# Kernel optimization log

Hardware: AMD Instinct MI355X
Metric: run time of the kernel (lower is better)

The kernel has to match this reference:

```python
import jax, jax.numpy as jnp
import numpy as np

NT = 128          # num_timesteps (reference query points)
E = 128           # embed_time
H = 128           # nhidden
NH = 1            # num_heads
F = 32            # feature_size
NS = 2            # num_states
EPS = 1e-5


def layer_norm(x, g, b):
    m = jnp.mean(x, axis=-1, keepdims=True)
    v = jnp.mean((x - m) ** 2, axis=-1, keepdims=True)
    return (x - m) * jax.lax.rsqrt(v + EPS) * g + b


def setup_inputs() -> dict:
    key = jax.random.key(0)
    ks = jax.random.split(key, 24)
    nrm = lambda k, s: (jax.random.normal(k, s) * 0.05).astype(jnp.float32)
    inp = {
        "input": jax.random.normal(ks[0], (8, F, 512), dtype=jnp.float32),
        "mask": jax.random.randint(ks[1], (8, F, 512), 0, 2).astype(jnp.float32),
        "timesteps": jnp.sort(jax.random.uniform(ks[2], (8, 512), dtype=jnp.float32), axis=-1),
        # time embedding
        "periodic_w": nrm(ks[3], (E - 1, 1)), "periodic_b": nrm(ks[4], (E - 1,)),
        "lin_w": nrm(ks[5], (1, 1)), "lin_b": nrm(ks[6], (1,)),
        # query / key projections + layer norms
        "q_w": nrm(ks[7], (E, E)), "q_b": nrm(ks[8], (E,)),
        "q_g": jnp.ones((E,), jnp.float32), "q_be": jnp.zeros((E,), jnp.float32),
        "k_w": nrm(ks[9], (E, E)), "k_b": nrm(ks[10], (E,)),
        "k_g": jnp.ones((E,), jnp.float32), "k_be": jnp.zeros((E,), jnp.float32),
        # attention_norm over h*2F channels, then output linear + LN to nhidden
        "attn_g": jnp.ones((NH * 2 * F,), jnp.float32), "attn_b": jnp.zeros((NH * 2 * F,), jnp.float32),
        "out_w": nrm(ks[11], (H, NH * 2 * F)), "out_b": nrm(ks[12], (H,)),
        "out_g": jnp.ones((H,), jnp.float32), "out_be": jnp.zeros((H,), jnp.float32),
        # GRU (torch gate order r, z, n)
        "gru_wih": nrm(ks[13], (3 * H, H)), "gru_whh": nrm(ks[14], (3 * H, H)),
        "gru_bih": nrm(ks[15], (3 * H,)), "gru_bhh": nrm(ks[16], (3 * H,)),
        # classifier MLP
        "c1_w": nrm(ks[17], (H, H)), "c1_b": nrm(ks[18], (H,)),
        "c2_w": nrm(ks[19], (H, H)), "c2_b": nrm(ks[20], (H,)),
        "c3_w": nrm(ks[21], (NS, H)), "c3_b": nrm(ks[22], (NS,)),
    }
    return inp


def time_embedding(tt, lin_w, lin_b, periodic_w, periodic_b):
    t = tt[..., None]                                   # (..., 1)
    out1 = t @ lin_w.T + lin_b                          # (..., 1)
    out2 = jnp.sin(t @ periodic_w.T + periodic_b)       # (..., E-1)
    return jnp.concatenate([out1, out2], axis=-1)       # (..., E)


def reference(input, mask, timesteps, periodic_w, periodic_b, lin_w, lin_b,
              q_w, q_b, q_g, q_be, k_w, k_b, k_g, k_be,
              attn_g, attn_b, out_w, out_b, out_g, out_be,
              gru_wih, gru_whh, gru_bih, gru_bhh,
              c1_w, c1_b, c2_w, c2_b, c3_w, c3_b):
    B = input.shape[0]
    x_in = jnp.transpose(input, (0, 2, 1))              # (B, T, F)
    m = 1.0 - jnp.transpose(mask, (0, 2, 1))            # (B, T, F)
    x_in = x_in * (m > 0).astype(x_in.dtype)
    x = jnp.concatenate([x_in, m], axis=-1)             # (B, T, 2F)
    mk = jnp.concatenate([m, m], axis=-1)               # (B, T, 2F)

    key_e = time_embedding(timesteps, lin_w, lin_b, periodic_w, periodic_b)        # (B, T, E)
    qtimes = jnp.linspace(0.0, 1.0, NT)
    query_e = time_embedding(qtimes[None], lin_w, lin_b, periodic_w, periodic_b)   # (1, NT, E)

    q = layer_norm(query_e @ q_w.T + q_b, q_g, q_be)    # (1, NT, E)
    k = layer_norm(key_e @ k_w.T + k_b, k_g, k_be)      # (B, T, E)

    etk = E // NH
    q = q.reshape(1, NT, NH, etk).transpose(0, 2, 1, 3)         # (1, h, NT, etk)
    k = k.reshape(B, -1, NH, etk).transpose(0, 2, 1, 3)         # (B, h, T, etk)

    scores = jnp.einsum("ahqd,bhkd->bhqk", q, k) / np.sqrt(etk)  # (B, h, NT, T)
    # per-channel masked softmax over keys: (B, h, NT, T, 2F)
    logits = jnp.where(mk[:, None, None, :, :] == 0, -1e9, scores[..., None])
    p_attn = jax.nn.softmax(logits, axis=-2)
    att = jnp.sum(p_attn * x[:, None, None, :, :], axis=-2)     # (B, h, NT, 2F)

    x2 = att.transpose(0, 2, 1, 3).reshape(B, NT, NH * 2 * F)
    x2 = layer_norm(x2, attn_g, attn_b)
    out = layer_norm(x2 @ out_w.T + out_b, out_g, out_be)       # (B, NT, H)

    # GRU over the NT reference timesteps, last hidden state
    seq = out.transpose(1, 0, 2)                                # (NT, B, H)
    h0 = jnp.zeros((B, H), out.dtype)

    def gru_step(h, x_t):
        gi = x_t @ gru_wih.T + gru_bih
        gh = h @ gru_whh.T + gru_bhh
        ir, iz, inn = jnp.split(gi, 3, axis=-1)
        hr, hz, hn = jnp.split(gh, 3, axis=-1)
        r = jax.nn.sigmoid(ir + hr)
        z = jax.nn.sigmoid(iz + hz)
        n = jnp.tanh(inn + r * hn)
        h_new = (1.0 - z) * n + z * h
        return h_new, None

    h_last, _ = jax.lax.scan(gru_step, h0, seq)

    h1 = jax.nn.relu(h_last @ c1_w.T + c1_b)
    h2 = jax.nn.relu(h1 @ c2_w.T + c2_b)
    return h2 @ c3_w.T + c3_b                                   # (B, num_states) logits
```

## Files before the change

kernel.cpp:

```cpp
#include <hip/hip_runtime.h>
#include <math.h>

#define LN_EPS 1e-5f

typedef _Float16 h2v __attribute__((ext_vector_type(2)));

__device__ __forceinline__ float dot4(float4 a, float4 b) {
    return a.x*b.x + a.y*b.y + a.z*b.z + a.w*b.w;
}
__device__ __forceinline__ void fma4(float4& a, float s, float4 v) {
    a.x += s*v.x; a.y += s*v.y; a.z += s*v.z; a.w += s*v.w;
}
__device__ __forceinline__ float fast_rcp(float x) {
    return __builtin_amdgcn_rcpf(x);
}
__device__ __forceinline__ float fast_sigmoid(float x) {
    return fast_rcp(1.f + __expf(-x));
}
__device__ __forceinline__ float fast_tanh(float x) {
    return 1.f - 2.f*fast_rcp(__expf(2.f*x) + 1.f);
}
__device__ __forceinline__ float fdot2u(unsigned int a, unsigned int b, float c) {
#if __has_builtin(__builtin_amdgcn_fdot2)
    return __builtin_amdgcn_fdot2(__builtin_bit_cast(h2v, a),
                                  __builtin_bit_cast(h2v, b), c, false);
#else
    const h2v av = __builtin_bit_cast(h2v, a);
    const h2v bv = __builtin_bit_cast(h2v, b);
    return c + (float)av[0]*(float)bv[0] + (float)av[1]*(float)bv[1];
#endif
}
__device__ __forceinline__ float wsum64(float v) {
    #pragma unroll
    for (int off = 32; off > 0; off >>= 1) v += __shfl_xor(v, off);
    return v;
}

__global__ void k_embed_proj(
    const float* __restrict__ input, const float* __restrict__ mask,
    const float* __restrict__ timesteps,
    const float* __restrict__ pw, const float* __restrict__ pb,
    const float* __restrict__ lw, const float* __restrict__ lb,
    const float* __restrict__ q_w, const float* __restrict__ q_b,
    const float* __restrict__ q_g, const float* __restrict__ q_be,
    const float* __restrict__ k_w, const float* __restrict__ k_b,
    const float* __restrict__ k_g, const float* __restrict__ k_be,
    float* __restrict__ qs, float* __restrict__ kT, float2* __restrict__ xm)
{
    const int blk = blockIdx.x;
    const int tid = threadIdx.x;

    __shared__ __align__(16) float e[4][128];
    __shared__ __align__(16) float4 red[128];
    __shared__ __align__(16) float proj[4][128];
    __shared__ __align__(16) float2 tile[32][65];

    if (blk < 64) {
        const int b  = blk >> 3;
        const int t0 = (blk & 7) * 64;
        const int cg = tid >> 6;
        const int tt = tid & 63;
        #pragma unroll
        for (int c16 = 0; c16 < 16; ++c16) {
            const int c = c16*2 + cg;
            const float m = mask [(size_t)(b*32 + c)*512 + t0 + tt];
            const float x = input[(size_t)(b*32 + c)*512 + t0 + tt];
            const float mm = 1.0f - m;
            tile[c][tt] = make_float2(x*mm, mm);
        }
        __syncthreads();
        const int c2 = tid & 31;
        const int tg = tid >> 5;
        #pragma unroll
        for (int k = 0; k < 16; ++k) {
            const int t = tg*16 + k;
            xm[((size_t)b*512 + t0 + t)*32 + c2] = tile[c2][t];
        }
        return;
    }

    const bool isq = blk < 96;
    float tv[4];
    int kidx0 = 0;
    if (isq) {
        const int q0 = (blk - 64) * 4;
        #pragma unroll
        for (int r = 0; r < 4; ++r) tv[r] = (float)(q0 + r) * (1.0f/127.0f);
    } else {
        kidx0 = (blk - 96) * 4;
        #pragma unroll
        for (int r = 0; r < 4; ++r) tv[r] = timesteps[kidx0 + r];
    }

    float pwj = 0.f, pbj = 0.f;
    if (tid > 0) { pwj = pw[tid-1]; pbj = pb[tid-1]; }
    const float lw0 = lw[0], lb0 = lb[0];
    #pragma unroll
    for (int r = 0; r < 4; ++r)
        e[r][tid] = (tid == 0) ? (tv[r]*lw0 + lb0) : sinf(tv[r]*pwj + pbj);
    __syncthreads();

    const float* W  = isq ? q_w  : k_w;
    const float* Bv = isq ? q_b  : k_b;
    const float* G  = isq ? q_g  : k_g;
    const float* Be = isq ? q_be : k_be;

    {
        const int jj = tid >> 2, dc = tid & 3;
        const float4* e0 = (const float4*)(&e[0][0]);
        const float4* e1 = (const float4*)(&e[1][0]);
        const float4* e2 = (const float4*)(&e[2][0]);
        const float4* e3 = (const float4*)(&e[3][0]);
        #pragma unroll
        for (int jb = 0; jb < 4; ++jb) {
            const int j = jb*32 + jj;
            const float4* wrow = (const float4*)(W + (size_t)j*128);
            float a0=0.f, a1=0.f, a2=0.f, a3=0.f;
            #pragma unroll
            for (int k = 0; k < 8; ++k) {
                const int idx = dc + 4*k;
                const float4 w4 = wrow[idx];
                a0 += dot4(w4, e0[idx]);
                a1 += dot4(w4, e1[idx]);
                a2 += dot4(w4, e2[idx]);
                a3 += dot4(w4, e3[idx]);
            }
            a0 += __shfl_xor(a0, 1, 4); a0 += __shfl_xor(a0, 2, 4);
            a1 += __shfl_xor(a1, 1, 4); a1 += __shfl_xor(a1, 2, 4);
            a2 += __shfl_xor(a2, 1, 4); a2 += __shfl_xor(a2, 2, 4);
            a3 += __shfl_xor(a3, 1, 4); a3 += __shfl_xor(a3, 2, 4);
            if (dc == 0) {
                const float bj = Bv[j];
                proj[0][j] = a0 + bj; proj[1][j] = a1 + bj;
                proj[2][j] = a2 + bj; proj[3][j] = a3 + bj;
            }
        }
    }
    __syncthreads();

    float acc[4];
    #pragma unroll
    for (int r = 0; r < 4; ++r) acc[r] = proj[r][tid];

    red[tid] = make_float4(acc[0], acc[1], acc[2], acc[3]);
    __syncthreads();
    for (int s = 64; s > 0; s >>= 1) {
        if (tid < s) {
            float4 m = red[tid]; const float4 o = red[tid+s];
            m.x += o.x; m.y += o.y; m.z += o.z; m.w += o.w;
            red[tid] = m;
        }
        __syncthreads();
    }
    float4 mean = red[0];
    mean.x *= (1.0f/128.0f); mean.y *= (1.0f/128.0f);
    mean.z *= (1.0f/128.0f); mean.w *= (1.0f/128.0f);
    __syncthreads();
    const float d0 = acc[0]-mean.x, d1 = acc[1]-mean.y,
                d2 = acc[2]-mean.z, d3 = acc[3]-mean.w;
    red[tid] = make_float4(d0*d0, d1*d1, d2*d2, d3*d3);
    __syncthreads();
    for (int s = 64; s > 0; s >>= 1) {
        if (tid < s) {
            float4 m = red[tid]; const float4 o = red[tid+s];
            m.x += o.x; m.y += o.y; m.z += o.z; m.w += o.w;
            red[tid] = m;
        }
        __syncthreads();
    }
    float4 var = red[0];
    var.x *= (1.0f/128.0f); var.y *= (1.0f/128.0f);
    var.z *= (1.0f/128.0f); var.w *= (1.0f/128.0f);

    const float gg = G[tid], bb = Be[tid];
    const float o0 = d0*rsqrtf(var.x+LN_EPS)*gg + bb;
    const float o1 = d1*rsqrtf(var.y+LN_EPS)*gg + bb;
    const float o2 = d2*rsqrtf(var.z+LN_EPS)*gg + bb;
    const float o3 = d3*rsqrtf(var.w+LN_EPS)*gg + bb;

    if (isq) {
        const float sc = 0.08838834764831845f;
        const int q0 = (blk - 64)*4;
        qs[(size_t)(q0+0)*128 + tid] = o0*sc;
        qs[(size_t)(q0+1)*128 + tid] = o1*sc;
        qs[(size_t)(q0+2)*128 + tid] = o2*sc;
        qs[(size_t)(q0+3)*128 + tid] = o3*sc;
    } else {
        const int b = kidx0 >> 9;
        const int t = kidx0 & 511;
        *(float4*)(kT + ((size_t)(b*128 + tid))*512 + t) =
            make_float4(o0, o1, o2, o3);
    }
}

__global__ void __launch_bounds__(256) k_attn(
    const float2* __restrict__ xm,
    const float* __restrict__ qs, const float* __restrict__ kT,
    const float* __restrict__ attn_g, const float* __restrict__ attn_b,
    const float* __restrict__ out_w, const float* __restrict__ out_b,
    const float* __restrict__ out_g, const float* __restrict__ out_be,
    float* __restrict__ outm)
{
    const int b     = blockIdx.x >> 5;
    const int qbase = (blockIdx.x & 31) * 4;
    const int tid   = threadIdx.x;

    __shared__ __align__(16) float et[4][512];
    __shared__ __align__(16) float qsh[4][128];
    __shared__ __align__(16) float wsh[128*66];
    __shared__ __align__(16) float sA[4][8][32];
    __shared__ __align__(16) float aA[4][8][32];
    __shared__ __align__(16) float x2s[4][64];
    __shared__ float redC[4];

    for (int idx = tid; idx < 512; idx += 256)
        qsh[idx >> 7][idx & 127] = qs[(size_t)(qbase + (idx >> 7))*128 + (idx & 127)];
    for (int idx = tid; idx < 8192; idx += 256)
        wsh[(idx >> 6)*66 + (idx & 63)] = out_w[idx];
    __syncthreads();

    {
        const int grp = tid >> 7;
        const int tl  = tid & 127;
        const int q0  = grp*2;
        const float4* kp  = (const float4*)kT + (size_t)b*128*128 + tl;
        const float4* qa4 = (const float4*)qsh[q0];
        const float4* qb4 = (const float4*)qsh[q0+1];
        float4 a0 = make_float4(0,0,0,0), a1 = make_float4(0,0,0,0);
        float4 c0 = kp[0], c1 = kp[128], c2 = kp[256], c3 = kp[384];
        for (int c = 0; c < 32; ++c) {
            float4 n0, n1, n2, n3;
            if (c < 31) {
                const float4* kn = kp + (size_t)(4*c+4)*128;
                n0 = kn[0]; n1 = kn[128]; n2 = kn[256]; n3 = kn[384];
            }
            const float4 qa = qa4[c], qb = qb4[c];
            fma4(a0, qa.x, c0); fma4(a1, qb.x, c0);
            fma4(a0, qa.y, c1); fma4(a1, qb.y, c1);
            fma4(a0, qa.z, c2); fma4(a1, qb.z, c2);
            fma4(a0, qa.w, c3); fma4(a1, qb.w, c3);
            c0 = n0; c1 = n1; c2 = n2; c3 = n3;
        }
        a0.x = __expf(a0.x); a0.y = __expf(a0.y); a0.z = __expf(a0.z); a0.w = __expf(a0.w);
        a1.x = __expf(a1.x); a1.y = __expf(a1.y); a1.z = __expf(a1.z); a1.w = __expf(a1.w);
        ((float4*)et[q0])[tl]   = a0;
        ((float4*)et[q0+1])[tl] = a1;
    }
    __syncthreads();

    {
        const int c   = tid & 31;
        const int seg = tid >> 5;
        const float2* xp = xm + ((size_t)b*512 + seg*64)*32 + c;
        float s0=0,s1=0,s2=0,s3=0, a0=0,a1=0,a2=0,a3=0;
        #pragma unroll 4
        for (int i = 0; i < 64; ++i) {
            const float2 v = xp[(size_t)i*32];
            const int t = seg*64 + i;
            const float w0 = et[0][t]*v.y, w1 = et[1][t]*v.y;
            const float w2 = et[2][t]*v.y, w3 = et[3][t]*v.y;
            s0 += w0; s1 += w1; s2 += w2; s3 += w3;
            a0 += w0*v.x; a1 += w1*v.x; a2 += w2*v.x; a3 += w3*v.x;
        }
        sA[0][seg][c]=s0; sA[1][seg][c]=s1; sA[2][seg][c]=s2; sA[3][seg][c]=s3;
        aA[0][seg][c]=a0; aA[1][seg][c]=a1; aA[2][seg][c]=a2; aA[3][seg][c]=a3;
    }
    __syncthreads();

    {
        const int ql = tid >> 6;
        const int c2 = tid & 63;
        const int cc = c2 & 31;
        float ss = 0.f;
        #pragma unroll
        for (int g = 0; g < 8; ++g) ss += sA[ql][g][cc];
        float attv;
        if (c2 < 32) {
            float aa = 0.f;
            #pragma unroll
            for (int g = 0; g < 8; ++g) aa += aA[ql][g][cc];
            attv = (ss > 0.f) ? aa/ss : 0.f;
        } else {
            attv = (ss > 0.f) ? 1.0f : 0.0f;
        }
        const float mean = wsum64(attv) * (1.0f/64.0f);
        const float dv = attv - mean;
        const float var = wsum64(dv*dv) * (1.0f/64.0f);
        x2s[ql][c2] = dv*rsqrtf(var+LN_EPS)*attn_g[c2] + attn_b[c2];
    }
    __syncthreads();

    {
        const int jhalf = tid >> 7;
        const int j     = tid & 127;
        const int wave  = tid >> 6;
        for (int lq2 = 0; lq2 < 2; ++lq2) {
            const int ql = jhalf*2 + lq2;
            float acc = out_b[j];
            const float4* wrow = (const float4*)(wsh + j*66);
            const float4* xr   = (const float4*)x2s[ql];
            #pragma unroll
            for (int k = 0; k < 16; ++k) acc += dot4(wrow[k], xr[k]);

            float v = wsum64(acc);
            if ((tid & 63) == 0) redC[wave] = v;
            __syncthreads();
            const float mean = (redC[jhalf*2] + redC[jhalf*2+1]) * (1.0f/128.0f);
            __syncthreads();
            const float d = acc - mean;
            v = wsum64(d*d);
            if ((tid & 63) == 0) redC[wave] = v;
            __syncthreads();
            const float var = (redC[jhalf*2] + redC[jhalf*2+1]) * (1.0f/128.0f);
            outm[((size_t)b*128 + qbase + ql)*128 + j] =
                d*rsqrtf(var+LN_EPS)*out_g[j] + out_be[j];
            __syncthreads();
        }
    }
}

__global__ void k_gi(const float* __restrict__ outm,
                     const float* __restrict__ wih, const float* __restrict__ bih,
                     float* __restrict__ gi)
{
    const int qi  = blockIdx.x;
    const int tid = threadIdx.x;
    __shared__ __align__(16) float rows[8][128];
    for (int idx = tid; idx < 1024; idx += 384) {
        const int b = idx >> 7, d = idx & 127;
        rows[b][d] = outm[(size_t)(b*128+qi)*128 + d];
    }
    __syncthreads();

    const int g0 = tid >> 2, dc = tid & 3;
    #pragma unroll
    for (int gb = 0; gb < 4; ++gb) {
        const int g = gb*96 + g0;
        const float4* wrow = (const float4*)(wih + (size_t)g*128);
        float acc[8] = {0,0,0,0,0,0,0,0};
        #pragma unroll
        for (int k = 0; k < 8; ++k) {
            const int idx = dc + 4*k;
            const float4 w4 = wrow[idx];
            #pragma unroll
            for (int b = 0; b < 8; ++b)
                acc[b] += dot4(w4, ((const float4*)rows[b])[idx]);
        }
        #pragma unroll
        for (int b = 0; b < 8; ++b) {
            acc[b] += __shfl_xor(acc[b], 1, 4);
            acc[b] += __shfl_xor(acc[b], 2, 4);
        }
        if (dc == 0) {
            const float bi = bih[g];
            #pragma unroll
            for (int b = 0; b < 8; ++b)
                gi[((size_t)qi*8 + b)*384 + g] = acc[b] + bi;
        }
    }
}

__global__ void __launch_bounds__(512) k_gru_cls(
    const float* __restrict__ gi,
    const float* __restrict__ whh, const float* __restrict__ bhh,
    const float* __restrict__ c1w, const float* __restrict__ c1b,
    const float* __restrict__ c2w, const float* __restrict__ c2b,
    const float* __restrict__ c3w, const float* __restrict__ c3b,
    float* __restrict__ out)
{
    const int b   = blockIdx.x;
    const int tid = threadIdx.x;
    const int s   = tid >> 7;
    const int u   = tid & 127;

    __shared__ __align__(16) unsigned int lds[25344];
    unsigned int* hP = lds;
    float4* part4 = (float4*)&lds[64];
    float* hcls = (float*)&lds[64 + 1536];

    {
        const float4* w4 = (const float4*)whh;
        #pragma unroll 4
        for (int k = 0; k < 24; ++k) {
            const int idx = tid + k*512;
            const float4 v = w4[idx];
            const int row = idx >> 5, c4 = idx & 31;
            h2v p0; p0[0] = (_Float16)v.x; p0[1] = (_Float16)v.y;
            h2v p1; p1[0] = (_Float16)v.z; p1[1] = (_Float16)v.w;
            lds[row*66 + c4*2    ] = __builtin_bit_cast(unsigned int, p0);
            lds[row*66 + c4*2 + 1] = __builtin_bit_cast(unsigned int, p1);
        }
    }
    __syncthreads();

    unsigned int wreg[3][16];
    #pragma unroll
    for (int g = 0; g < 3; ++g) {
        const uint2* src = (const uint2*)&lds[(g*128 + u)*66 + 16*s];
        #pragma unroll
        for (int i = 0; i < 8; ++i) {
            const uint2 t = src[i];
            wreg[g][2*i] = t.x; wreg[g][2*i+1] = t.y;
        }
    }
    __syncthreads();

    const float* gbase = gi + (size_t)b*384;
    float bh_r=0.f, bh_z=0.f, bh_n=0.f, gr0=0.f, gz0=0.f, gn0=0.f, hprev=0.f;
    if (tid < 64) hP[tid] = 0u;
    if (s == 0) {
        bh_r = bhh[u]; bh_z = bhh[u+128]; bh_n = bhh[u+256];
        gr0 = gbase[u]; gz0 = gbase[u+128]; gn0 = gbase[u+256];
    }
    __syncthreads();

    for (int qi = 0; qi < 128; ++qi) {
        const uint4* hp4 = (const uint4*)hP + s*4;
        float ar = 0.f, az = 0.f, an = 0.f;
        #pragma unroll
        for (int i = 0; i < 4; ++i) {
            const uint4 hv = hp4[i];
            ar = fdot2u(wreg[0][4*i+0], hv.x, ar);
            ar = fdot2u(wreg[0][4*i+1], hv.y, ar);
            ar = fdot2u(wreg[0][4*i+2], hv.z, ar);
            ar = fdot2u(wreg[0][4*i+3], hv.w, ar);
            az = fdot2u(wreg[1][4*i+0], hv.x, az);
            az = fdot2u(wreg[1][4*i+1], hv.y, az);
            az = fdot2u(wreg[1][4*i+2], hv.z, az);
            az = fdot2u(wreg[1][4*i+3], hv.w, az);
            an = fdot2u(wreg[2][4*i+0], hv.x, an);
            an = fdot2u(wreg[2][4*i+1], hv.y, an);
            an = fdot2u(wreg[2][4*i+2], hv.z, an);
            an = fdot2u(wreg[2][4*i+3], hv.w, an);
        }
        if (s > 0) part4[(s-1)*128 + u] = make_float4(ar, az, an, 0.f);

        float grn=0.f, gzn=0.f, gnn=0.f;
        if (s == 0 && qi < 127) {
            const float* gb = gbase + (size_t)(qi+1)*3072;
            grn = gb[u]; gzn = gb[u+128]; gnn = gb[u+256];
        }
        __syncthreads();

        if (s == 0) {
            const float4 p0 = part4[u], p1 = part4[128+u], p2 = part4[256+u];
            const float ghr = ar + p0.x + p1.x + p2.x + bh_r;
            const float ghz = az + p0.y + p1.y + p2.y + bh_z;
            const float ghn = an + p0.z + p1.z + p2.z + bh_n;
            const float r = fast_sigmoid(gr0 + ghr);
            const float z = fast_sigmoid(gz0 + ghz);
            const float n = fast_tanh(gn0 + r*ghn);
            const float hn2 = (1.f - z)*n + z*hprev;
            hprev = hn2;
            gr0 = grn; gz0 = gzn; gn0 = gnn;
            const float other = __shfl_xor(hn2, 1);
            if ((u & 1) == 0) {
                h2v hp; hp[0] = (_Float16)hn2; hp[1] = (_Float16)other;
                hP[u >> 1] = __builtin_bit_cast(unsigned int, hp);
            }
        }
        __syncthreads();
    }

    float* scr = (float*)part4;
    if (s == 0) hcls[u] = hprev;
    __syncthreads();
    if (tid < 128) {
        float acc = c1b[u];
        const float4* wc = (const float4*)(c1w + (size_t)u*128);
        const float4* v  = (const float4*)hcls;
        #pragma unroll
        for (int d4 = 0; d4 < 32; ++d4) acc += dot4(wc[d4], v[d4]);
        scr[u] = fmaxf(acc, 0.f);
    }
    __syncthreads();
    if (tid < 128) {
        float acc = c2b[u];
        const float4* wc = (const float4*)(c2w + (size_t)u*128);
        const float4* v  = (const float4*)scr;
        #pragma unroll
        for (int d4 = 0; d4 < 32; ++d4) acc += dot4(wc[d4], v[d4]);
        scr[128 + u] = fmaxf(acc, 0.f);
    }
    __syncthreads();
    if (tid < 2) {
        float acc = c3b[tid];
        const float4* wc = (const float4*)(c3w + (size_t)tid*128);
        const float4* v  = (const float4*)(scr + 128);
        #pragma unroll
        for (int d4 = 0; d4 < 32; ++d4) acc += dot4(wc[d4], v[d4]);
        out[(size_t)b*2 + tid] = acc;
    }
}

extern "C" void kernel_launch(void* const* d_in, const int* in_sizes, int n_in,
                              void* d_out, int out_size, void* d_ws, size_t ws_size,
                              hipStream_t stream)
{
    const float* input     = (const float*)d_in[0];
    const float* mask      = (const float*)d_in[1];
    const float* timesteps = (const float*)d_in[2];
    const float* pw        = (const float*)d_in[3];
    const float* pb        = (const float*)d_in[4];
    const float* lw        = (const float*)d_in[5];
    const float* lb        = (const float*)d_in[6];
    const float* q_w       = (const float*)d_in[7];
    const float* q_b       = (const float*)d_in[8];
    const float* q_g       = (const float*)d_in[9];
    const float* q_be      = (const float*)d_in[10];
    const float* k_w       = (const float*)d_in[11];
    const float* k_b       = (const float*)d_in[12];
    const float* k_g       = (const float*)d_in[13];
    const float* k_be      = (const float*)d_in[14];
    const float* attn_g    = (const float*)d_in[15];
    const float* attn_b    = (const float*)d_in[16];
    const float* out_w     = (const float*)d_in[17];
    const float* out_b     = (const float*)d_in[18];
    const float* out_g     = (const float*)d_in[19];
    const float* out_be    = (const float*)d_in[20];
    const float* gru_wih   = (const float*)d_in[21];
    const float* gru_whh   = (const float*)d_in[22];
    const float* gru_bih   = (const float*)d_in[23];
    const float* gru_bhh   = (const float*)d_in[24];
    const float* c1_w      = (const float*)d_in[25];
    const float* c1_b      = (const float*)d_in[26];
    const float* c2_w      = (const float*)d_in[27];
    const float* c2_b      = (const float*)d_in[28];
    const float* c3_w      = (const float*)d_in[29];
    const float* c3_b      = (const float*)d_in[30];

    float* ws   = (float*)d_ws;
    float*  qs   = ws;
    float*  kT   = qs   + 16384;
    float*  outm = kT   + 524288;
    float*  gi   = outm + 131072;
    float2* xm   = (float2*)(gi + 393216);

    k_embed_proj<<<1120, 128, 0, stream>>>(input, mask, timesteps,
                                           pw, pb, lw, lb,
                                           q_w, q_b, q_g, q_be,
                                           k_w, k_b, k_g, k_be, qs, kT, xm);
    k_attn<<<256, 256, 0, stream>>>(xm, qs, kT,
                                    attn_g, attn_b, out_w, out_b,
                                    out_g, out_be, outm);
    k_gi<<<128, 384, 0, stream>>>(outm, gru_wih, gru_bih, gi);
    k_gru_cls<<<8, 512, 0, stream>>>(gi, gru_whh, gru_bhh,
                                     c1_w, c1_b, c2_w, c2_b, c3_w, c3_b,
                                     (float*)d_out);
}
```

Baseline: 240.5 us.

## Run GRU recurrence with one thread per hidden unit and double-buffered state

```diff
diff --git a/kernel.cpp b/kernel.cpp
--- a/kernel.cpp
+++ b/kernel.cpp
@@ -360,7 +360,7 @@
     }
 }
 
-__global__ void __launch_bounds__(512) k_gru_cls(
+__global__ void __launch_bounds__(128) k_gru_cls(
     const float* __restrict__ gi,
     const float* __restrict__ whh, const float* __restrict__ bhh,
     const float* __restrict__ c1w, const float* __restrict__ c1b,
@@ -368,21 +368,19 @@
     const float* __restrict__ c3w, const float* __restrict__ c3b,
     float* __restrict__ out)
 {
-    const int b   = blockIdx.x;
-    const int tid = threadIdx.x;
-    const int s   = tid >> 7;
-    const int u   = tid & 127;
+    const int b = blockIdx.x;
+    const int u = threadIdx.x;
 
     __shared__ __align__(16) unsigned int lds[25344];
-    unsigned int* hP = lds;
-    float4* part4 = (float4*)&lds[64];
-    float* hcls = (float*)&lds[64 + 1536];
+    unsigned int* hP  = lds;
+    float* hcls = (float*)&lds[192];
+    float* scr  = (float*)&lds[320];
 
     {
         const float4* w4 = (const float4*)whh;
         #pragma unroll 4
-        for (int k = 0; k < 24; ++k) {
-            const int idx = tid + k*512;
+        for (int k = 0; k < 96; ++k) {
+            const int idx = u + k*128;
             const float4 v = w4[idx];
             const int row = idx >> 5, c4 = idx & 31;
             h2v p0; p0[0] = (_Float16)v.x; p0[1] = (_Float16)v.y;
@@ -393,79 +391,70 @@
     }
     __syncthreads();
 
-    unsigned int wreg[3][16];
-    #pragma unroll
-    for (int g = 0; g < 3; ++g) {
-        const uint2* src = (const uint2*)&lds[(g*128 + u)*66 + 16*s];
-        #pragma unroll
-        for (int i = 0; i < 8; ++i) {
-            const uint2 t = src[i];
-            wreg[g][2*i] = t.x; wreg[g][2*i+1] = t.y;
+    unsigned int wr_[64], wz_[64], wn_[64];
+    {
+        const uint2* sr = (const uint2*)&lds[(size_t)u*66];
+        const uint2* sz = (const uint2*)&lds[(size_t)(u+128)*66];
+        const uint2* sn = (const uint2*)&lds[(size_t)(u+256)*66];
+        #pragma unroll
+        for (int i = 0; i < 32; ++i) {
+            const uint2 a = sr[i]; wr_[2*i] = a.x; wr_[2*i+1] = a.y;
+            const uint2 c = sz[i]; wz_[2*i] = c.x; wz_[2*i+1] = c.y;
+            const uint2 d = sn[i]; wn_[2*i] = d.x; wn_[2*i+1] = d.y;
         }
     }
     __syncthreads();
 
     const float* gbase = gi + (size_t)b*384;
-    float bh_r=0.f, bh_z=0.f, bh_n=0.f, gr0=0.f, gz0=0.f, gn0=0.f, hprev=0.f;
-    if (tid < 64) hP[tid] = 0u;
-    if (s == 0) {
-        bh_r = bhh[u]; bh_z = bhh[u+128]; bh_n = bhh[u+256];
-        gr0 = gbase[u]; gz0 = gbase[u+128]; gn0 = gbase[u+256];
-    }
-    __syncthreads();
-
+    const float bh_r = bhh[u], bh_z = bhh[u+128], bh_n = bhh[u+256];
+    float gr0 = gbase[u], gz0 = gbase[u+128], gn0 = gbase[u+256];
+    float hprev = 0.f;
+    if (u < 64) hP[u] = 0u;
+    __syncthreads();
+
+    int p = 0;
     for (int qi = 0; qi < 128; ++qi) {
-        const uint4* hp4 = (const uint4*)hP + s*4;
+        const uint4* hp4 = (const uint4*)(hP + p*64);
         float ar = 0.f, az = 0.f, an = 0.f;
         #pragma unroll
-        for (int i = 0; i < 4; ++i) {
+        for (int i = 0; i < 16; ++i) {
             const uint4 hv = hp4[i];
-            ar = fdot2u(wreg[0][4*i+0], hv.x, ar);
-            ar = fdot2u(wreg[0][4*i+1], hv.y, ar);
-            ar = fdot2u(wreg[0][4*i+2], hv.z, ar);
-            ar = fdot2u(wreg[0][4*i+3], hv.w, ar);
-            az = fdot2u(wreg[1][4*i+0], hv.x, az);
-            az = fdot2u(wreg[1][4*i+1], hv.y, az);
-            az = fdot2u(wreg[1][4*i+2], hv.z, az);
-            az = fdot2u(wreg[1][4*i+3], hv.w, az);
-            an = fdot2u(wreg[2][4*i+0], hv.x, an);
-            an = fdot2u(wreg[2][4*i+1], hv.y, an);
-            an = fdot2u(wreg[2][4*i+2], hv.z, an);
-            an = fdot2u(wreg[2][4*i+3], hv.w, an);
-        }
-        if (s > 0) part4[(s-1)*128 + u] = make_float4(ar, az, an, 0.f);
-
-        float grn=0.f, gzn=0.f, gnn=0.f;
-        if (s == 0 && qi < 127) {
+            ar = fdot2u(wr_[4*i+0], hv.x, ar);
+            ar = fdot2u(wr_[4*i+1], hv.y, ar);
+            ar = fdot2u(wr_[4*i+2], hv.z, ar);
+            ar = fdot2u(wr_[4*i+3], hv.w, ar);
+            az = fdot2u(wz_[4*i+0], hv.x, az);
+            az = fdot2u(wz_[4*i+1], hv.y, az);
+            az = fdot2u(wz_[4*i+2], hv.z, az);
+            az = fdot2u(wz_[4*i+3], hv.w, az);
+            an = fdot2u(wn_[4*i+0], hv.x, an);
+            an = fdot2u(wn_[4*i+1], hv.y, an);
+            an = fdot2u(wn_[4*i+2], hv.z, an);
+            an = fdot2u(wn_[4*i+3], hv.w, an);
+        }
+
+        float grn = 0.f, gzn = 0.f, gnn = 0.f;
+        if (qi < 127) {
             const float* gb = gbase + (size_t)(qi+1)*3072;
             grn = gb[u]; gzn = gb[u+128]; gnn = gb[u+256];
         }
+
+        const float r = fast_sigmoid(gr0 + ar + bh_r);
+        const float z = fast_sigmoid(gz0 + az + bh_z);
+        const float n = fast_tanh(gn0 + r*(an + bh_n));
+        const float hn2 = (1.f - z)*n + z*hprev;
+        hprev = hn2;
+        gr0 = grn; gz0 = gzn; gn0 = gnn;
+
+        _Float16* hw = (_Float16*)(hP + (1-p)*64);
+        hw[u] = (_Float16)hn2;
         __syncthreads();
-
-        if (s == 0) {
-            const float4 p0 = part4[u], p1 = part4[128+u], p2 = part4[256+u];
-            const float ghr = ar + p0.x + p1.x + p2.x + bh_r;
-            const float ghz = az + p0.y + p1.y + p2.y + bh_z;
-            const float ghn = an + p0.z + p1.z + p2.z + bh_n;
-            const float r = fast_sigmoid(gr0 + ghr);
-            const float z = fast_sigmoid(gz0 + ghz);
-            const float n = fast_tanh(gn0 + r*ghn);
-            const float hn2 = (1.f - z)*n + z*hprev;
-            hprev = hn2;
-            gr0 = grn; gz0 = gzn; gn0 = gnn;
-            const float other = __shfl_xor(hn2, 1);
-            if ((u & 1) == 0) {
-                h2v hp; hp[0] = (_Float16)hn2; hp[1] = (_Float16)other;
-                hP[u >> 1] = __builtin_bit_cast(unsigned int, hp);
-            }
-        }
-        __syncthreads();
-    }
-
-    float* scr = (float*)part4;
-    if (s == 0) hcls[u] = hprev;
-    __syncthreads();
-    if (tid < 128) {
+        p ^= 1;
+    }
+
+    hcls[u] = hprev;
+    __syncthreads();
+    {
         float acc = c1b[u];
         const float4* wc = (const float4*)(c1w + (size_t)u*128);
         const float4* v  = (const float4*)hcls;
@@ -474,7 +463,7 @@
         scr[u] = fmaxf(acc, 0.f);
     }
     __syncthreads();
-    if (tid < 128) {
+    {
         float acc = c2b[u];
         const float4* wc = (const float4*)(c2w + (size_t)u*128);
         const float4* v  = (const float4*)scr;
@@ -483,13 +472,13 @@
         scr[128 + u] = fmaxf(acc, 0.f);
     }
     __syncthreads();
-    if (tid < 2) {
-        float acc = c3b[tid];
-        const float4* wc = (const float4*)(c3w + (size_t)tid*128);
+    if (u < 2) {
+        float acc = c3b[u];
+        const float4* wc = (const float4*)(c3w + (size_t)u*128);
         const float4* v  = (const float4*)(scr + 128);
         #pragma unroll
         for (int d4 = 0; d4 < 32; ++d4) acc += dot4(wc[d4], v[d4]);
-        out[(size_t)b*2 + tid] = acc;
+        out[(size_t)b*2 + u] = acc;
     }
 }
 
@@ -544,7 +533,7 @@
                                     attn_g, attn_b, out_w, out_b,
                                     out_g, out_be, outm);
     k_gi<<<128, 384, 0, stream>>>(outm, gru_wih, gru_bih, gi);
-    k_gru_cls<<<8, 512, 0, stream>>>(gi, gru_whh, gru_bhh,
+    k_gru_cls<<<8, 128, 0, stream>>>(gi, gru_whh, gru_bhh,
                                      c1_w, c1_b, c2_w, c2_b, c3_w, c3_b,
                                      (float*)d_out);
 }
```

Measured after the change: 248.8 us. +3.5%, slower.

## Prefetch all GRU input-gate values into LDS as fp16 before the recurrence

Applied to the files above, without the earlier changes.

```diff
diff --git a/kernel.cpp b/kernel.cpp
--- a/kernel.cpp
+++ b/kernel.cpp
@@ -29,6 +29,10 @@
     const h2v bv = __builtin_bit_cast(h2v, b);
     return c + (float)av[0]*(float)bv[0] + (float)av[1]*(float)bv[1];
 #endif
+}
+__device__ __forceinline__ float half_of(unsigned int w, int hi) {
+    const h2v p = __builtin_bit_cast(h2v, w);
+    return (float)p[hi];
 }
 __device__ __forceinline__ float wsum64(float v) {
     #pragma unroll
@@ -373,10 +377,9 @@
     const int s   = tid >> 7;
     const int u   = tid & 127;
 
-    __shared__ __align__(16) unsigned int lds[25344];
-    unsigned int* hP = lds;
-    float4* part4 = (float4*)&lds[64];
-    float* hcls = (float*)&lds[64 + 1536];
+    __shared__ __align__(16) unsigned int lds[25984];
+    unsigned int* hP    = lds + 24384;
+    float4*       part4 = (float4*)(lds + 24448);
 
     {
         const float4* w4 = (const float4*)whh;
@@ -405,15 +408,27 @@
     }
     __syncthreads();
 
+    {
+        const float* gb0 = gi;
+        for (int idx = tid; idx < 24384; idx += 512) {
+            const int q1 = idx / 192;
+            const int pr = idx - q1*192;
+            const float2 v = *(const float2*)(gb0 +
+                ((size_t)(q1+1)*8 + b)*384 + 2*pr);
+            h2v pk; pk[0] = (_Float16)v.x; pk[1] = (_Float16)v.y;
+            lds[idx] = __builtin_bit_cast(unsigned int, pk);
+        }
+    }
     const float* gbase = gi + (size_t)b*384;
     float bh_r=0.f, bh_z=0.f, bh_n=0.f, gr0=0.f, gz0=0.f, gn0=0.f, hprev=0.f;
-    if (tid < 64) hP[tid] = 0u;
-    if (s == 0) {
+    if (tid < 128) {
         bh_r = bhh[u]; bh_z = bhh[u+128]; bh_n = bhh[u+256];
         gr0 = gbase[u]; gz0 = gbase[u+128]; gn0 = gbase[u+256];
     }
-    __syncthreads();
-
+    if (tid < 64) hP[tid] = 0u;
+    __syncthreads();
+
+    const int uh = u >> 1, up = u & 1;
     for (int qi = 0; qi < 128; ++qi) {
         const uint4* hp4 = (const uint4*)hP + s*4;
         float ar = 0.f, az = 0.f, an = 0.f;
@@ -436,13 +451,15 @@
         if (s > 0) part4[(s-1)*128 + u] = make_float4(ar, az, an, 0.f);
 
         float grn=0.f, gzn=0.f, gnn=0.f;
-        if (s == 0 && qi < 127) {
-            const float* gb = gbase + (size_t)(qi+1)*3072;
-            grn = gb[u]; gzn = gb[u+128]; gnn = gb[u+256];
+        if (tid < 128 && qi < 127) {
+            const unsigned int* gq = lds + (size_t)qi*192;
+            grn = half_of(gq[uh],       up);
+            gzn = half_of(gq[64 + uh],  up);
+            gnn = half_of(gq[128 + uh], up);
         }
         __syncthreads();
 
-        if (s == 0) {
+        if (tid < 128) {
             const float4 p0 = part4[u], p1 = part4[128+u], p2 = part4[256+u];
             const float ghr = ar + p0.x + p1.x + p2.x + bh_r;
             const float ghz = az + p0.y + p1.y + p2.y + bh_z;
@@ -453,17 +470,14 @@
             const float hn2 = (1.f - z)*n + z*hprev;
             hprev = hn2;
             gr0 = grn; gz0 = gzn; gn0 = gnn;
-            const float other = __shfl_xor(hn2, 1);
-            if ((u & 1) == 0) {
-                h2v hp; hp[0] = (_Float16)hn2; hp[1] = (_Float16)other;
-                hP[u >> 1] = __builtin_bit_cast(unsigned int, hp);
-            }
+            ((_Float16*)hP)[u] = (_Float16)hn2;
         }
         __syncthreads();
     }
 
-    float* scr = (float*)part4;
-    if (s == 0) hcls[u] = hprev;
+    float* hcls = (float*)lds;
+    float* scr  = (float*)lds + 128;
+    if (tid < 128) hcls[u] = hprev;
     __syncthreads();
     if (tid < 128) {
         float acc = c1b[u];
```

New measurement: 246.3 us. 2.4% more time.

## Pack GRU input gates as fp16 pairs and prefetch them into LDS

Applied to the files above, without the earlier changes.

```diff
diff --git a/kernel.cpp b/kernel.cpp
--- a/kernel.cpp
+++ b/kernel.cpp
@@ -29,6 +29,10 @@
     const h2v bv = __builtin_bit_cast(h2v, b);
     return c + (float)av[0]*(float)bv[0] + (float)av[1]*(float)bv[1];
 #endif
+}
+__device__ __forceinline__ float half_of(unsigned int w, int hi) {
+    const h2v p = __builtin_bit_cast(h2v, w);
+    return (float)p[hi];
 }
 __device__ __forceinline__ float wsum64(float v) {
     #pragma unroll
@@ -321,7 +325,7 @@
 
 __global__ void k_gi(const float* __restrict__ outm,
                      const float* __restrict__ wih, const float* __restrict__ bih,
-                     float* __restrict__ gi)
+                     unsigned int* __restrict__ gi3)
 {
     const int qi  = blockIdx.x;
     const int tid = threadIdx.x;
@@ -346,22 +350,30 @@
             for (int b = 0; b < 8; ++b)
                 acc[b] += dot4(w4, ((const float4*)rows[b])[idx]);
         }
+        const float bi = bih[g];
         #pragma unroll
         for (int b = 0; b < 8; ++b) {
             acc[b] += __shfl_xor(acc[b], 1, 4);
             acc[b] += __shfl_xor(acc[b], 2, 4);
-        }
-        if (dc == 0) {
-            const float bi = bih[g];
-            #pragma unroll
-            for (int b = 0; b < 8; ++b)
-                gi[((size_t)qi*8 + b)*384 + g] = acc[b] + bi;
-        }
-    }
-}
-
-__global__ void __launch_bounds__(512) k_gru_cls(
-    const float* __restrict__ gi,
+            acc[b] += bi;
+        }
+        const bool writer = (dc == 0) && ((g & 1) == 0);
+        const int v    = (g & 127) >> 1;
+        const int gate = g >> 7;
+        #pragma unroll
+        for (int b = 0; b < 8; ++b) {
+            const float pB = __shfl_xor(acc[b], 4);
+            if (writer) {
+                h2v pk; pk[0] = (_Float16)acc[b]; pk[1] = (_Float16)pB;
+                gi3[((size_t)qi*8 + b)*192 + v*3 + gate] =
+                    __builtin_bit_cast(unsigned int, pk);
+            }
+        }
+    }
+}
+
+__global__ void __launch_bounds__(256) k_gru_cls(
+    const unsigned int* __restrict__ gi3,
     const float* __restrict__ whh, const float* __restrict__ bhh,
     const float* __restrict__ c1w, const float* __restrict__ c1b,
     const float* __restrict__ c2w, const float* __restrict__ c2b,
@@ -370,125 +382,172 @@
 {
     const int b   = blockIdx.x;
     const int tid = threadIdx.x;
-    const int s   = tid >> 7;
-    const int u   = tid & 127;
-
-    __shared__ __align__(16) unsigned int lds[25344];
-    unsigned int* hP = lds;
-    float4* part4 = (float4*)&lds[64];
-    float* hcls = (float*)&lds[64 + 1536];
+    const int s   = tid >> 6;
+    const int v   = tid & 63;
+
+    __shared__ __align__(16) unsigned int lds[25984];
+    unsigned int* giL = lds;
+    unsigned int* hP  = lds + 24384;
+    float2* part2     = (float2*)(lds + 24448);
+    float* hcls       = (float*)(lds + 25600);
+    float* scr        = (float*)(lds + 25728);
 
     {
         const float4* w4 = (const float4*)whh;
         #pragma unroll 4
-        for (int k = 0; k < 24; ++k) {
-            const int idx = tid + k*512;
-            const float4 v = w4[idx];
+        for (int k = 0; k < 48; ++k) {
+            const int idx = tid + k*256;
+            const float4 val = w4[idx];
             const int row = idx >> 5, c4 = idx & 31;
-            h2v p0; p0[0] = (_Float16)v.x; p0[1] = (_Float16)v.y;
-            h2v p1; p1[0] = (_Float16)v.z; p1[1] = (_Float16)v.w;
+            h2v p0; p0[0] = (_Float16)val.x; p0[1] = (_Float16)val.y;
+            h2v p1; p1[0] = (_Float16)val.z; p1[1] = (_Float16)val.w;
             lds[row*66 + c4*2    ] = __builtin_bit_cast(unsigned int, p0);
             lds[row*66 + c4*2 + 1] = __builtin_bit_cast(unsigned int, p1);
         }
     }
     __syncthreads();
 
-    unsigned int wreg[3][16];
-    #pragma unroll
-    for (int g = 0; g < 3; ++g) {
-        const uint2* src = (const uint2*)&lds[(g*128 + u)*66 + 16*s];
-        #pragma unroll
-        for (int i = 0; i < 8; ++i) {
-            const uint2 t = src[i];
-            wreg[g][2*i] = t.x; wreg[g][2*i+1] = t.y;
-        }
-    }
-    __syncthreads();
-
-    const float* gbase = gi + (size_t)b*384;
-    float bh_r=0.f, bh_z=0.f, bh_n=0.f, gr0=0.f, gz0=0.f, gn0=0.f, hprev=0.f;
+    unsigned int w6[6][16];
+    {
+        const int rows6[6] = { 2*v, 2*v+1, 128+2*v, 129+2*v, 256+2*v, 257+2*v };
+        #pragma unroll
+        for (int r = 0; r < 6; ++r) {
+            const uint2* src = (const uint2*)&lds[rows6[r]*66 + s*16];
+            #pragma unroll
+            for (int i = 0; i < 8; ++i) {
+                const uint2 t = src[i];
+                w6[r][2*i] = t.x; w6[r][2*i+1] = t.y;
+            }
+        }
+    }
+    __syncthreads();
+
+    for (int idx = tid; idx < 24384; idx += 256) {
+        const int q1 = idx / 192;
+        const int j  = idx - q1*192;
+        giL[idx] = gi3[((size_t)(q1+1)*8 + b)*192 + j];
+    }
+
+    float bhrA=0.f,bhrB=0.f,bhzA=0.f,bhzB=0.f,bhnA=0.f,bhnB=0.f;
+    if (s == 1) {
+        bhrA = bhh[2*v];     bhrB = bhh[2*v+1];
+        bhzA = bhh[128+2*v]; bhzB = bhh[129+2*v];
+        bhnA = bhh[256+2*v]; bhnB = bhh[257+2*v];
+    }
+    unsigned int gu0=0u, gu1=0u, gu2=0u;
+    float hprevA = 0.f, hprevB = 0.f;
+    if (s == 0) {
+        const unsigned int* g0p = gi3 + (size_t)b*192 + v*3;
+        gu0 = g0p[0]; gu1 = g0p[1]; gu2 = g0p[2];
+    }
     if (tid < 64) hP[tid] = 0u;
-    if (s == 0) {
-        bh_r = bhh[u]; bh_z = bhh[u+128]; bh_n = bhh[u+256];
-        gr0 = gbase[u]; gz0 = gbase[u+128]; gn0 = gbase[u+256];
-    }
     __syncthreads();
 
     for (int qi = 0; qi < 128; ++qi) {
         const uint4* hp4 = (const uint4*)hP + s*4;
-        float ar = 0.f, az = 0.f, an = 0.f;
+        float arA=0.f, arB=0.f, azA=0.f, azB=0.f, anA=0.f, anB=0.f;
         #pragma unroll
         for (int i = 0; i < 4; ++i) {
             const uint4 hv = hp4[i];
-            ar = fdot2u(wreg[0][4*i+0], hv.x, ar);
-            ar = fdot2u(wreg[0][4*i+1], hv.y, ar);
-            ar = fdot2u(wreg[0][4*i+2], hv.z, ar);
-            ar = fdot2u(wreg[0][4*i+3], hv.w, ar);
-            az = fdot2u(wreg[1][4*i+0], hv.x, az);
-            az = fdot2u(wreg[1][4*i+1], hv.y, az);
-            az = fdot2u(wreg[1][4*i+2], hv.z, az);
-            az = fdot2u(wreg[1][4*i+3], hv.w, az);
-            an = fdot2u(wreg[2][4*i+0], hv.x, an);
-            an = fdot2u(wreg[2][4*i+1], hv.y, an);
-            an = fdot2u(wreg[2][4*i+2], hv.z, an);
-            an = fdot2u(wreg[2][4*i+3], hv.w, an);
-        }
-        if (s > 0) part4[(s-1)*128 + u] = make_float4(ar, az, an, 0.f);
-
-        float grn=0.f, gzn=0.f, gnn=0.f;
+            arA = fdot2u(w6[0][4*i+0], hv.x, arA);
+            arA = fdot2u(w6[0][4*i+1], hv.y, arA);
+            arA = fdot2u(w6[0][4*i+2], hv.z, arA);
+            arA = fdot2u(w6[0][4*i+3], hv.w, arA);
+            arB = fdot2u(w6[1][4*i+0], hv.x, arB);
+            arB = fdot2u(w6[1][4*i+1], hv.y, arB);
+            arB = fdot2u(w6[1][4*i+2], hv.z, arB);
+            arB = fdot2u(w6[1][4*i+3], hv.w, arB);
+            azA = fdot2u(w6[2][4*i+0], hv.x, azA);
+            azA = fdot2u(w6[2][4*i+1], hv.y, azA);
+            azA = fdot2u(w6[2][4*i+2], hv.z, azA);
+            azA = fdot2u(w6[2][4*i+3], hv.w, azA);
+            azB = fdot2u(w6[3][4*i+0], hv.x, azB);
+            azB = fdot2u(w6[3][4*i+1], hv.y, azB);
+            azB = fdot2u(w6[3][4*i+2], hv.z, azB);
+            azB = fdot2u(w6[3][4*i+3], hv.w, azB);
+            anA = fdot2u(w6[4][4*i+0], hv.x, anA);
+            anA = fdot2u(w6[4][4*i+1], hv.y, anA);
+            anA = fdot2u(w6[4][4*i+2], hv.z, anA);
+            anA = fdot2u(w6[4][4*i+3], hv.w, anA);
+            anB = fdot2u(w6[5][4*i+0], hv.x, anB);
+            anB = fdot2u(w6[5][4*i+1], hv.y, anB);
+            anB = fdot2u(w6[5][4*i+2], hv.z, anB);
+            anB = fdot2u(w6[5][4*i+3], hv.w, anB);
+        }
+        if (s == 1) {
+            arA += bhrA; arB += bhrB; azA += bhzA; azB += bhzB;
+            anA += bhnA; anB += bhnB;
+        }
+        if (s > 0) {
+            float2* p = part2 + (s-1)*192;
+            p[v]       = make_float2(arA, arB);
+            p[64 + v]  = make_float2(azA, azB);
+            p[128 + v] = make_float2(anA, anB);
+        }
+
+        unsigned int gn0=0u, gn1=0u, gn2=0u;
         if (s == 0 && qi < 127) {
-            const float* gb = gbase + (size_t)(qi+1)*3072;
-            grn = gb[u]; gzn = gb[u+128]; gnn = gb[u+256];
+            const unsigned int* gq = giL + (size_t)qi*192 + v*3;
+            gn0 = gq[0]; gn1 = gq[1]; gn2 = gq[2];
         }
         __syncthreads();
 
         if (s == 0) {
-            const float4 p0 = part4[u], p1 = part4[128+u], p2 = part4[256+u];
-            const float ghr = ar + p0.x + p1.x + p2.x + bh_r;
-            const float ghz = az + p0.y + p1.y + p2.y + bh_z;
-            const float ghn = an + p0.z + p1.z + p2.z + bh_n;
-            const float r = fast_sigmoid(gr0 + ghr);
-            const float z = fast_sigmoid(gz0 + ghz);
-            const float n = fast_tanh(gn0 + r*ghn);
-            const float hn2 = (1.f - z)*n + z*hprev;
-            hprev = hn2;
-            gr0 = grn; gz0 = gzn; gn0 = gnn;
-            const float other = __shfl_xor(hn2, 1);
-            if ((u & 1) == 0) {
-                h2v hp; hp[0] = (_Float16)hn2; hp[1] = (_Float16)other;
-                hP[u >> 1] = __builtin_bit_cast(unsigned int, hp);
+            float ghrA = arA, ghrB = arB, ghzA = azA, ghzB = azB,
+                  ghnA = anA, ghnB = anB;
+            #pragma unroll
+            for (int sl = 0; sl < 3; ++sl) {
+                const float2 pr = part2[sl*192 + v];
+                const float2 pz = part2[sl*192 + 64 + v];
+                const float2 pn = part2[sl*192 + 128 + v];
+                ghrA += pr.x; ghrB += pr.y;
+                ghzA += pz.x; ghzB += pz.y;
+                ghnA += pn.x; ghnB += pn.y;
             }
+            const float rA = fast_sigmoid(half_of(gu0,0) + ghrA);
+            const float rB = fast_sigmoid(half_of(gu0,1) + ghrB);
+            const float zA = fast_sigmoid(half_of(gu1,0) + ghzA);
+            const float zB = fast_sigmoid(half_of(gu1,1) + ghzB);
+            const float nA = fast_tanh(half_of(gu2,0) + rA*ghnA);
+            const float nB = fast_tanh(half_of(gu2,1) + rB*ghnB);
+            const float hA = (1.f - zA)*nA + zA*hprevA;
+            const float hB = (1.f - zB)*nB + zB*hprevB;
+            hprevA = hA; hprevB = hB;
+            gu0 = gn0; gu1 = gn1; gu2 = gn2;
+            h2v hp; hp[0] = (_Float16)hA; hp[1] = (_Float16)hB;
+            hP[v] = __builtin_bit_cast(unsigned int, hp);
         }
         __syncthreads();
     }
 
-    float* scr = (float*)part4;
-    if (s == 0) hcls[u] = hprev;
+    if (s == 0) { hcls[2*v] = hprevA; hcls[2*v+1] = hprevB; }
     __syncthreads();
     if (tid < 128) {
+        const int u = tid;
         float acc = c1b[u];
         const float4* wc = (const float4*)(c1w + (size_t)u*128);
-        const float4* v  = (const float4*)hcls;
-        #pragma unroll
-        for (int d4 = 0; d4 < 32; ++d4) acc += dot4(wc[d4], v[d4]);
+        const float4* vv = (const float4*)hcls;
+        #pragma unroll
+        for (int d4 = 0; d4 < 32; ++d4) acc += dot4(wc[d4], vv[d4]);
         scr[u] = fmaxf(acc, 0.f);
     }
     __syncthreads();
     if (tid < 128) {
+        const int u = tid;
         float acc = c2b[u];
         const float4* wc = (const float4*)(c2w + (size_t)u*128);
-        const float4* v  = (const float4*)scr;
-        #pragma unroll
-        for (int d4 = 0; d4 < 32; ++d4) acc += dot4(wc[d4], v[d4]);
+        const float4* vv = (const float4*)scr;
+        #pragma unroll
+        for (int d4 = 0; d4 < 32; ++d4) acc += dot4(wc[d4], vv[d4]);
         scr[128 + u] = fmaxf(acc, 0.f);
     }
     __syncthreads();
     if (tid < 2) {
         float acc = c3b[tid];
         const float4* wc = (const float4*)(c3w + (size_t)tid*128);
-        const float4* v  = (const float4*)(scr + 128);
-        #pragma unroll
-        for (int d4 = 0; d4 < 32; ++d4) acc += dot4(wc[d4], v[d4]);
+        const float4* vv = (const float4*)(scr + 128);
+        #pragma unroll
+        for (int d4 = 0; d4 < 32; ++d4) acc += dot4(wc[d4], vv[d4]);
         out[(size_t)b*2 + tid] = acc;
     }
 }
@@ -533,8 +592,8 @@
     float*  qs   = ws;
     float*  kT   = qs   + 16384;
     float*  outm = kT   + 524288;
-    float*  gi   = outm + 131072;
-    float2* xm   = (float2*)(gi + 393216);
+    unsigned int* gi3 = (unsigned int*)(outm + 131072);
+    float2* xm   = (float2*)(outm + 131072 + 196608);
 
     k_embed_proj<<<1120, 128, 0, stream>>>(input, mask, timesteps,
                                            pw, pb, lw, lb,
@@ -543,8 +602,8 @@
     k_attn<<<256, 256, 0, stream>>>(xm, qs, kT,
                                     attn_g, attn_b, out_w, out_b,
                                     out_g, out_be, outm);
-    k_gi<<<128, 384, 0, stream>>>(outm, gru_wih, gru_bih, gi);
-    k_gru_cls<<<8, 512, 0, stream>>>(gi, gru_whh, gru_bhh,
+    k_gi<<<128, 384, 0, stream>>>(outm, gru_wih, gru_bih, gi3);
+    k_gru_cls<<<8, 256, 0, stream>>>(gi3, gru_whh, gru_bhh,
                                      c1_w, c1_b, c2_w, c2_b, c3_w, c3_b,
                                      (float*)d_out);
 }
```

Measured after the change: 261.5 us. 1.09x slower.
